# Optimization experiments

Hardware: AMD Instinct MI355X
Metric: run time of the kernel (lower is better)

Reference implementation:

```python
import jax, jax.numpy as jnp
import numpy as np

NUM_USERS = 4096
NUM_ITEMS = 8192
EMBED_DIM = 64
NUM_LAYERS = 3


def setup_inputs() -> dict:
    key = jax.random.key(0)
    k1, k2 = jax.random.split(key)
    # embedding table for users+items (nn.Embedding init normal std=0.1)
    x = jax.random.normal(k1, (NUM_USERS + NUM_ITEMS, EMBED_DIM), dtype=jnp.float32) * 0.1
    # dense 0/1 user-item interaction matrix (forward applies torch.nonzero to it)
    edge_index = jax.random.randint(k2, (NUM_USERS, NUM_ITEMS), 0, 2, dtype=jnp.int32)
    return {"x": x, "edge_index": edge_index}


def reference(x, edge_index):
    U, I, L = NUM_USERS, NUM_ITEMS, NUM_LAYERS
    adj = edge_index.astype(jnp.float32)  # [U, I], 0/1
    # symmetric degree normalization: adj / sqrt(deg_u * deg_i), nan (0/0) -> 0
    deg_u = jnp.sum(adj, axis=1)  # [U]
    deg_i = jnp.sum(adj, axis=0)  # [I]
    denom = jnp.sqrt(deg_u[:, None] * deg_i[None, :])  # [U, I]
    weights = jnp.where(denom > 0, adj / jnp.where(denom > 0, denom, 1.0), 0.0)
    # weights is identical every layer (depends only on edge_index)
    acc = jnp.zeros_like(x)
    for _ in range(L):
        # NOTE: original code concatenates (item-side, user-side) in this order
        x = jnp.concatenate([weights.T @ x[:U], weights @ x[U:]], axis=0)  # [I+U, d]
        acc = acc + x
    # alpha = 1/(1+L) * ones applied to every layer output
    return acc / (1.0 + L)
```

## Files before the change

kernel.cpp:

```cpp
#include <hip/hip_runtime.h>

#define NU 4096
#define NI 8192
#define ND 64
#define NTOT 12288
#define CT 8
#define CB 16
#define BROW 520

typedef unsigned short u16;
typedef unsigned int u32;
typedef unsigned long long u64;

__device__ __forceinline__ u16 f2bf(float f) {
    union { float f; u32 u; } v; v.f = f;
    u32 u = v.u;
    u += 0x7FFFu + ((u >> 16) & 1u);
    return (u16)(u >> 16);
}

typedef short frag8 __attribute__((ext_vector_type(8)));
typedef float f32x4 __attribute__((ext_vector_type(4)));

__global__ __launch_bounds__(256) void k_pack2(const int* __restrict__ edge,
        u64* __restrict__ Apk, u64* __restrict__ ATpk) {
    __shared__ __align__(16) u16 At[256][40];
    __shared__ __align__(16) u64 Tt[512][6];
    const int t = threadIdx.x;
    const int u0 = (blockIdx.x >> 4) * 256;
    const int i0 = (blockIdx.x & 15) * 512;
    const int cg = t & 31;
    const int rb = t >> 5;

    #pragma unroll 4
    for (int rr = 0; rr < 32; rr++) {
        const int row = rb * 32 + rr;
        const int4* p = (const int4*)(edge + (size_t)(u0 + row) * NI + i0 + cg * 16);
        u32 bits = 0;
        #pragma unroll
        for (int m = 0; m < 4; m++) {
            int4 v = p[m];
            bits |= (v.x != 0 ? 1u : 0u) << (m * 4 + 0);
            bits |= (v.y != 0 ? 1u : 0u) << (m * 4 + 1);
            bits |= (v.z != 0 ? 1u : 0u) << (m * 4 + 2);
            bits |= (v.w != 0 ? 1u : 0u) << (m * 4 + 3);
        }
        At[row][cg] = (u16)bits;
    }
    __syncthreads();

    {
        u64* dst = Apk + (size_t)(u0 + t) * 128 + (i0 >> 6);
        #pragma unroll
        for (int q = 0; q < 4; q++) {
            uint4 v = *(const uint4*)&At[t][q * 8];
            *(uint4*)(dst + q * 2) = v;
        }
    }

    {
        const int lane = t & 63, w = t >> 6;
        const u64 M[6] = {0x00000000FFFFFFFFULL, 0x0000FFFF0000FFFFULL,
                          0x00FF00FF00FF00FFULL, 0x0F0F0F0F0F0F0F0FULL,
                          0x3333333333333333ULL, 0x5555555555555555ULL};
        #pragma unroll
        for (int sc = 0; sc < 8; sc++) {
            u64 x = *(const u64*)&At[w * 64 + lane][sc * 4];
            #pragma unroll
            for (int si = 0; si < 6; si++) {
                const int s = 32 >> si;
                u64 y = __shfl_xor(x, s, 64);
                x = (lane & s) ? ((x & ~M[si]) | ((y >> s) & M[si]))
                               : ((x &  M[si]) | ((y << s) & ~M[si]));
            }
            Tt[sc * 64 + lane][w] = x;
        }
    }
    __syncthreads();
    #pragma unroll
    for (int j = 0; j < 2; j++) {
        const int item = t * 2 + j;
        ulonglong2 a = *(const ulonglong2*)&Tt[item][0];
        ulonglong2 b = *(const ulonglong2*)&Tt[item][2];
        u64* dst = ATpk + (size_t)(i0 + item) * 64 + (u0 >> 6);
        *(ulonglong2*)dst = a;
        *(ulonglong2*)(dst + 2) = b;
    }
}

__global__ __launch_bounds__(256) void k_scale0(const float* __restrict__ x,
        const u64* __restrict__ Apk, const u64* __restrict__ ATpk,
        float* __restrict__ dsu, float* __restrict__ dsi,
        u16* __restrict__ BuT, u16* __restrict__ BiT) {
    __shared__ float sc[64];
    const int t = threadIdx.x;
    const int r0 = blockIdx.x * 64;
    {
        const int rl = t >> 2, part = t & 3;
        int cnt = 0;
        if (r0 < NU) {
            const u64* p = Apk + (size_t)(r0 + rl) * 128 + part * 32;
            #pragma unroll
            for (int i = 0; i < 32; i++) cnt += (int)__popcll(p[i]);
        } else {
            const u64* p = ATpk + (size_t)(r0 - NU + rl) * 64 + part * 16;
            #pragma unroll
            for (int i = 0; i < 16; i++) cnt += (int)__popcll(p[i]);
        }
        cnt += __shfl_xor(cnt, 1, 64);
        cnt += __shfl_xor(cnt, 2, 64);
        if (part == 0) {
            float s = cnt > 0 ? rsqrtf((float)cnt) : 0.f;
            sc[rl] = s;
            if (r0 < NU) dsu[r0 + rl] = s; else dsi[r0 - NU + rl] = s;
        }
    }
    __syncthreads();
    const int r4 = t >> 4, c4 = t & 15;
    float y[4][4];
    #pragma unroll
    for (int j = 0; j < 4; j++) {
        const int rl = r4 * 4 + j;
        const float s = sc[rl];
        float4 xv = *(const float4*)(x + (size_t)(r0 + rl) * ND + c4 * 4);
        y[j][0] = xv.x * s; y[j][1] = xv.y * s;
        y[j][2] = xv.z * s; y[j][3] = xv.w * s;
    }
    u16* dst; size_t stride; int col0;
    if (r0 < NU) { dst = BuT; stride = NU; col0 = r0; }
    else         { dst = BiT; stride = NI; col0 = r0 - NU; }
    #pragma unroll
    for (int k = 0; k < 4; k++) {
        ushort4 w;
        w.x = f2bf(y[0][k]); w.y = f2bf(y[1][k]);
        w.z = f2bf(y[2][k]); w.w = f2bf(y[3][k]);
        *(ushort4*)(dst + (size_t)(c4 * 4 + k) * stride + col0 + r4 * 4) = w;
    }
}

__global__ __launch_bounds__(256) void k_gemm(
        const u64* __restrict__ Apk, const u64* __restrict__ ATpk,
        const u16* __restrict__ BuT, const u16* __restrict__ BiT,
        float* __restrict__ Ptop, float* __restrict__ Pbot) {
    __shared__ __align__(16) u16 Bs[64 * BROW];
    const int t = threadIdx.x, bx = blockIdx.x;
    const int lane = t & 63, w = t >> 6, lr = lane & 15, lg = lane >> 4;
    const u64* arow; const u16* dense; int Kstr, wpr, kbase, pstr; float* Pout;
    if (bx < 1024) {
        const int tile = bx >> 3, chunk = bx & 7;
        arow = ATpk + (size_t)(tile * 64) * 64 + chunk * 8; wpr = 64;
        dense = BuT; Kstr = NU; kbase = chunk * 512; pstr = CT * 64;
        Pout = Ptop + (size_t)(tile * 64) * pstr + chunk * 64;
    } else {
        const int b2 = bx - 1024, tile = b2 >> 4, chunk = b2 & 15;
        arow = Apk + (size_t)(tile * 64) * 128 + chunk * 8; wpr = 128;
        dense = BiT; Kstr = NI; kbase = chunk * 512; pstr = CB * 64;
        Pout = Pbot + (size_t)(tile * 64) * pstr + chunk * 64;
    }
    const u16* gsrc = dense + kbase;
    #pragma unroll
    for (int it = 0; it < 16; it++) {
        const int e = it * 4 + w;
        __builtin_amdgcn_global_load_lds(
            (const __attribute__((address_space(1))) void*)
                (gsrc + (size_t)e * Kstr + lane * 8),
            (__attribute__((address_space(3))) void*)(&Bs[e * BROW]),
            16, 0, 0);
    }
    const u64* myrow = arow + (size_t)(w * 16 + lr) * wpr;
    u64 aw[8];
    #pragma unroll
    for (int qq = 0; qq < 4; qq++) {
        ulonglong2 v = *(const ulonglong2*)(myrow + qq * 2);
        aw[qq * 2] = v.x; aw[qq * 2 + 1] = v.y;
    }
    f32x4 acc[4];
    #pragma unroll
    for (int i = 0; i < 4; i++) acc[i] = f32x4{0.f, 0.f, 0.f, 0.f};
    __syncthreads();

    #pragma unroll
    for (int kk = 0; kk < 8; kk++) {
        const u32 lo = (u32)aw[kk], hi = (u32)(aw[kk] >> 32);
        const u32 byte0 = (lo >> (lg * 8)) & 0xFFu;
        const u32 byte1 = (hi >> (lg * 8)) & 0xFFu;
        frag8 bf0, bf1;
        #pragma unroll
        for (int j = 0; j < 8; j++) {
            bf0[j] = (short)(((byte0 >> j) & 1u) ? 0x3F80 : 0);
            bf1[j] = (short)(((byte1 >> j) & 1u) ? 0x3F80 : 0);
        }
        #pragma unroll
        for (int nt = 0; nt < 4; nt++) {
            const int e = nt * 16 + lr;
            frag8 a0 = *(const frag8*)&Bs[e * BROW + kk * 64 + lg * 8];
            frag8 a1 = *(const frag8*)&Bs[e * BROW + kk * 64 + 32 + lg * 8];
            acc[nt] = __builtin_amdgcn_mfma_f32_16x16x32_bf16(a0, bf0, acc[nt], 0, 0, 0);
            acc[nt] = __builtin_amdgcn_mfma_f32_16x16x32_bf16(a1, bf1, acc[nt], 0, 0, 0);
        }
    }
    __syncthreads();
    float* Fs = (float*)Bs;
    #pragma unroll
    for (int nt = 0; nt < 4; nt++) {
        const int row = w * 16 + lr, g = nt * 4 + lg;
        *(f32x4*)&Fs[row * 64 + (((g + row) & 15) * 4)] = acc[nt];
    }
    __syncthreads();
    #pragma unroll
    for (int ii = 0; ii < 4; ii++) {
        const int slot = t + ii * 256;
        const int row = slot >> 4, g = slot & 15;
        f32x4 v = *(const f32x4*)&Fs[row * 64 + (((g + row) & 15) * 4)];
        *(f32x4*)&Pout[(size_t)row * pstr + g * 4] = v;
    }
}

__global__ __launch_bounds__(256) void k_reduce(
        const float* __restrict__ Ptop, const float* __restrict__ Pbot,
        const float* __restrict__ dsu, const float* __restrict__ dsi,
        float* __restrict__ accbuf, u16* __restrict__ BuTn,
        u16* __restrict__ BiTn, float* __restrict__ out, int layer) {
    __shared__ u16 TB[64][24];
    const int t = threadIdx.x, bx = blockIdx.x;
    const int rl = t >> 4, e4 = t & 15;
    int grow; float so;
    float sx = 0.f, sy = 0.f, sz = 0.f, sw = 0.f;
    if (bx < 512) {
        grow = bx * 16 + rl;
        const float* p = Ptop + (size_t)grow * (CT * 64) + e4 * 4;
        #pragma unroll
        for (int c = 0; c < CT; c++) {
            float4 v = *(const float4*)(p + c * 64);
            sx += v.x; sy += v.y; sz += v.z; sw += v.w;
        }
        so = dsi[grow];
    } else {
        const int u = (bx - 512) * 16 + rl;
        grow = NI + u;
        const float* p = Pbot + (size_t)u * (CB * 64) + e4 * 4;
        #pragma unroll
        for (int c = 0; c < CB; c++) {
            float4 v = *(const float4*)(p + c * 64);
            sx += v.x; sy += v.y; sz += v.z; sw += v.w;
        }
        so = dsu[grow - NI];
    }
    float4 y;
    y.x = sx * so; y.y = sy * so; y.z = sz * so; y.w = sw * so;
    const size_t o = (size_t)grow * ND + e4 * 4;
    if (layer == 0) {
        *(float4*)(accbuf + o) = y;
    } else if (layer == 1) {
        float4 a = *(const float4*)(accbuf + o);
        a.x += y.x; a.y += y.y; a.z += y.z; a.w += y.w;
        *(float4*)(accbuf + o) = a;
    } else {
        float4 a = *(const float4*)(accbuf + o);
        a.x = (a.x + y.x) * 0.25f; a.y = (a.y + y.y) * 0.25f;
        a.z = (a.z + y.z) * 0.25f; a.w = (a.w + y.w) * 0.25f;
        *(float4*)(out + o) = a;
    }
    if (layer != 2) {
        const float fn = (grow < NU) ? dsu[grow] : dsi[grow - NU];
        TB[e4 * 4 + 0][rl] = f2bf(y.x * fn);
        TB[e4 * 4 + 1][rl] = f2bf(y.y * fn);
        TB[e4 * 4 + 2][rl] = f2bf(y.z * fn);
        TB[e4 * 4 + 3][rl] = f2bf(y.w * fn);
        __syncthreads();
        if (t < 128) {
            const int e = t >> 1, h = t & 1;
            u16* dst; size_t stride; int col0;
            if (bx < 256)      { dst = BuTn; stride = NU; col0 = bx * 16; }
            else if (bx < 512) { dst = BiTn; stride = NI; col0 = bx * 16 - NU; }
            else               { dst = BiTn; stride = NI; col0 = (bx - 512) * 16 + NI - NU; }
            uint4 v = *(const uint4*)&TB[e][h * 8];
            *(uint4*)(dst + (size_t)e * stride + col0 + h * 8) = v;
        }
    }
}

extern "C" void kernel_launch(void* const* d_in, const int* in_sizes, int n_in,
                              void* d_out, int out_size, void* d_ws, size_t ws_size,
                              hipStream_t stream) {
    (void)in_sizes; (void)n_in; (void)out_size; (void)ws_size;
    const float* x    = (const float*)d_in[0];
    const int*   edge = (const int*)d_in[1];
    float* out = (float*)d_out;

    char* ws = (char*)d_ws;
    size_t off = 0;
    u64* Apk  = (u64*)(ws + off); off += (size_t)NU * (NI / 64) * 8;
    u64* ATpk = (u64*)(ws + off); off += (size_t)NI * (NU / 64) * 8;
    float* dsu = (float*)(ws + off); off += (size_t)NU * 4;
    float* dsi = (float*)(ws + off); off += (size_t)NI * 4;
    u16* BuT0 = (u16*)(ws + off); off += (size_t)ND * NU * 2;
    u16* BuT1 = (u16*)(ws + off); off += (size_t)ND * NU * 2;
    u16* BiT0 = (u16*)(ws + off); off += (size_t)ND * NI * 2;
    u16* BiT1 = (u16*)(ws + off); off += (size_t)ND * NI * 2;
    float* acc  = (float*)(ws + off); off += (size_t)NTOT * ND * 4;
    float* Ptop = (float*)(ws + off); off += (size_t)NI * CT * 64 * 4;
    float* Pbot = (float*)(ws + off); off += (size_t)NU * CB * 64 * 4;

    k_pack2<<<256, 256, 0, stream>>>(edge, Apk, ATpk);
    k_scale0<<<NTOT / 64, 256, 0, stream>>>(x, Apk, ATpk, dsu, dsi, BuT0, BiT0);

    k_gemm<<<2048, 256, 0, stream>>>(Apk, ATpk, BuT0, BiT0, Ptop, Pbot);
    k_reduce<<<768, 256, 0, stream>>>(Ptop, Pbot, dsu, dsi, acc, BuT1, BiT1, out, 0);
    k_gemm<<<2048, 256, 0, stream>>>(Apk, ATpk, BuT1, BiT1, Ptop, Pbot);
    k_reduce<<<768, 256, 0, stream>>>(Ptop, Pbot, dsu, dsi, acc, BuT0, BiT0, out, 1);
    k_gemm<<<2048, 256, 0, stream>>>(Apk, ATpk, BuT0, BiT0, Ptop, Pbot);
    k_reduce<<<768, 256, 0, stream>>>(Ptop, Pbot, dsu, dsi, acc,
                                      (u16*)nullptr, (u16*)nullptr, out, 2);
}
```

Measured before the change: 289.0 us.

## Compute 256 rows per GEMM block and expand adjacency bits via multiply trick

```diff
diff --git a/kernel.cpp b/kernel.cpp
--- a/kernel.cpp
+++ b/kernel.cpp
@@ -7,6 +7,8 @@
 #define CT 8
 #define CB 16
 #define BROW 520
+
+#define DSC 0.5f
 
 typedef unsigned short u16;
 typedef unsigned int u32;
@@ -121,7 +123,7 @@
     #pragma unroll
     for (int j = 0; j < 4; j++) {
         const int rl = r4 * 4 + j;
-        const float s = sc[rl];
+        const float s = sc[rl] * DSC;
         float4 xv = *(const float4*)(x + (size_t)(r0 + rl) * ND + c4 * 4);
         y[j][0] = xv.x * s; y[j][1] = xv.y * s;
         y[j][2] = xv.z * s; y[j][3] = xv.w * s;
@@ -138,24 +140,24 @@
     }
 }
 
-__global__ __launch_bounds__(256) void k_gemm(
+__global__ __launch_bounds__(256, 2) void k_gemm(
         const u64* __restrict__ Apk, const u64* __restrict__ ATpk,
         const u16* __restrict__ BuT, const u16* __restrict__ BiT,
         float* __restrict__ Ptop, float* __restrict__ Pbot) {
     __shared__ __align__(16) u16 Bs[64 * BROW];
     const int t = threadIdx.x, bx = blockIdx.x;
     const int lane = t & 63, w = t >> 6, lr = lane & 15, lg = lane >> 4;
-    const u64* arow; const u16* dense; int Kstr, wpr, kbase, pstr; float* Pout;
-    if (bx < 1024) {
+    const u64* abase; const u16* dense; int Kstr, wpr, kbase, pstr; float* Pout;
+    if (bx < 256) {
         const int tile = bx >> 3, chunk = bx & 7;
-        arow = ATpk + (size_t)(tile * 64) * 64 + chunk * 8; wpr = 64;
+        abase = ATpk + (size_t)(tile * 256) * 64 + chunk * 8; wpr = 64;
         dense = BuT; Kstr = NU; kbase = chunk * 512; pstr = CT * 64;
-        Pout = Ptop + (size_t)(tile * 64) * pstr + chunk * 64;
+        Pout = Ptop + (size_t)(tile * 256) * pstr + chunk * 64;
     } else {
-        const int b2 = bx - 1024, tile = b2 >> 4, chunk = b2 & 15;
-        arow = Apk + (size_t)(tile * 64) * 128 + chunk * 8; wpr = 128;
+        const int b2 = bx - 256, tile = b2 >> 4, chunk = b2 & 15;
+        abase = Apk + (size_t)(tile * 256) * 128 + chunk * 8; wpr = 128;
         dense = BiT; Kstr = NI; kbase = chunk * 512; pstr = CB * 64;
-        Pout = Pbot + (size_t)(tile * 64) * pstr + chunk * 64;
+        Pout = Pbot + (size_t)(tile * 256) * pstr + chunk * 64;
     }
     const u16* gsrc = dense + kbase;
     #pragma unroll
@@ -167,48 +169,65 @@
             (__attribute__((address_space(3))) void*)(&Bs[e * BROW]),
             16, 0, 0);
     }
-    const u64* myrow = arow + (size_t)(w * 16 + lr) * wpr;
-    u64 aw[8];
-    #pragma unroll
-    for (int qq = 0; qq < 4; qq++) {
-        ulonglong2 v = *(const ulonglong2*)(myrow + qq * 2);
-        aw[qq * 2] = v.x; aw[qq * 2 + 1] = v.y;
-    }
-    f32x4 acc[4];
-    #pragma unroll
-    for (int i = 0; i < 4; i++) acc[i] = f32x4{0.f, 0.f, 0.f, 0.f};
-    __syncthreads();
-
+    u64 aw[4][8];
+    #pragma unroll
+    for (int g = 0; g < 4; g++) {
+        const u64* myrow = abase + (size_t)(w * 64 + g * 16 + lr) * wpr;
+        #pragma unroll
+        for (int q = 0; q < 4; q++) {
+            ulonglong2 v = *(const ulonglong2*)(myrow + q * 2);
+            aw[g][q * 2] = v.x; aw[g][q * 2 + 1] = v.y;
+        }
+    }
+    f32x4 acc[4][4];
+    #pragma unroll
+    for (int g = 0; g < 4; g++)
+        #pragma unroll
+        for (int nt = 0; nt < 4; nt++) acc[g][nt] = f32x4{0.f, 0.f, 0.f, 0.f};
+    __syncthreads();
+
+    const int sh = lg * 8;
     #pragma unroll
     for (int kk = 0; kk < 8; kk++) {
-        const u32 lo = (u32)aw[kk], hi = (u32)(aw[kk] >> 32);
-        const u32 byte0 = (lo >> (lg * 8)) & 0xFFu;
-        const u32 byte1 = (hi >> (lg * 8)) & 0xFFu;
-        frag8 bf0, bf1;
-        #pragma unroll
-        for (int j = 0; j < 8; j++) {
-            bf0[j] = (short)(((byte0 >> j) & 1u) ? 0x3F80 : 0);
-            bf1[j] = (short)(((byte1 >> j) & 1u) ? 0x3F80 : 0);
-        }
+        #pragma unroll
+        for (int half = 0; half < 2; half++) {
+            frag8 bf[4];
+            #pragma unroll
+            for (int g = 0; g < 4; g++) {
+                const u32 b = (u32)(aw[g][kk] >> (sh + half * 32)) & 0xFFu;
+                const u64 p = (u64)b * 0x20004000ULL;
+                union { frag8 f; u32 u[4]; } bb;
+                bb.u[0] = ((u32)(p     )) & 0x40004000u;
+                bb.u[1] = ((u32)(p >> 2)) & 0x40004000u;
+                bb.u[2] = ((u32)(p >> 4)) & 0x40004000u;
+                bb.u[3] = ((u32)(p >> 6)) & 0x40004000u;
+                bf[g] = bb.f;
+            }
+            #pragma unroll
+            for (int nt = 0; nt < 4; nt++) {
+                frag8 a = *(const frag8*)
+                    &Bs[(nt * 16 + lr) * BROW + kk * 64 + half * 32 + sh];
+                #pragma unroll
+                for (int g = 0; g < 4; g++)
+                    acc[g][nt] = __builtin_amdgcn_mfma_f32_16x16x32_bf16(
+                        a, bf[g], acc[g][nt], 0, 0, 0);
+            }
+        }
+    }
+    __syncthreads();
+    float* Fs = (float*)Bs;
+    #pragma unroll
+    for (int g = 0; g < 4; g++) {
+        const int il = w * 64 + g * 16 + lr;
         #pragma unroll
         for (int nt = 0; nt < 4; nt++) {
-            const int e = nt * 16 + lr;
-            frag8 a0 = *(const frag8*)&Bs[e * BROW + kk * 64 + lg * 8];
-            frag8 a1 = *(const frag8*)&Bs[e * BROW + kk * 64 + 32 + lg * 8];
-            acc[nt] = __builtin_amdgcn_mfma_f32_16x16x32_bf16(a0, bf0, acc[nt], 0, 0, 0);
-            acc[nt] = __builtin_amdgcn_mfma_f32_16x16x32_bf16(a1, bf1, acc[nt], 0, 0, 0);
-        }
-    }
-    __syncthreads();
-    float* Fs = (float*)Bs;
-    #pragma unroll
-    for (int nt = 0; nt < 4; nt++) {
-        const int row = w * 16 + lr, g = nt * 4 + lg;
-        *(f32x4*)&Fs[row * 64 + (((g + row) & 15) * 4)] = acc[nt];
-    }
-    __syncthreads();
-    #pragma unroll
-    for (int ii = 0; ii < 4; ii++) {
+            const int gr = nt * 4 + lg;
+            *(f32x4*)&Fs[il * 64 + (((gr + il) & 15) * 4)] = acc[g][nt];
+        }
+    }
+    __syncthreads();
+    #pragma unroll
+    for (int ii = 0; ii < 16; ii++) {
         const int slot = t + ii * 256;
         const int row = slot >> 4, g = slot & 15;
         f32x4 v = *(const f32x4*)&Fs[row * 64 + (((g + row) & 15) * 4)];
@@ -262,7 +281,7 @@
         *(float4*)(out + o) = a;
     }
     if (layer != 2) {
-        const float fn = (grow < NU) ? dsu[grow] : dsi[grow - NU];
+        const float fn = ((grow < NU) ? dsu[grow] : dsi[grow - NU]) * DSC;
         TB[e4 * 4 + 0][rl] = f2bf(y.x * fn);
         TB[e4 * 4 + 1][rl] = f2bf(y.y * fn);
         TB[e4 * 4 + 2][rl] = f2bf(y.z * fn);
@@ -305,11 +324,11 @@
     k_pack2<<<256, 256, 0, stream>>>(edge, Apk, ATpk);
     k_scale0<<<NTOT / 64, 256, 0, stream>>>(x, Apk, ATpk, dsu, dsi, BuT0, BiT0);
 
-    k_gemm<<<2048, 256, 0, stream>>>(Apk, ATpk, BuT0, BiT0, Ptop, Pbot);
+    k_gemm<<<512, 256, 0, stream>>>(Apk, ATpk, BuT0, BiT0, Ptop, Pbot);
     k_reduce<<<768, 256, 0, stream>>>(Ptop, Pbot, dsu, dsi, acc, BuT1, BiT1, out, 0);
-    k_gemm<<<2048, 256, 0, stream>>>(Apk, ATpk, BuT1, BiT1, Ptop, Pbot);
+    k_gemm<<<512, 256, 0, stream>>>(Apk, ATpk, BuT1, BiT1, Ptop, Pbot);
     k_reduce<<<768, 256, 0, stream>>>(Ptop, Pbot, dsu, dsi, acc, BuT0, BiT0, out, 1);
-    k_gemm<<<2048, 256, 0, stream>>>(Apk, ATpk, BuT0, BiT0, Ptop, Pbot);
+    k_gemm<<<512, 256, 0, stream>>>(Apk, ATpk, BuT0, BiT0, Ptop, Pbot);
     k_reduce<<<768, 256, 0, stream>>>(Ptop, Pbot, dsu, dsi, acc,
                                       (u16*)nullptr, (u16*)nullptr, out, 2);
 }
```

Measured after the change: 273.0 us (median of 2 runs). 5.5% less time.
